# Performance work log

Hardware: AMD Instinct MI355X
Metric: run time of the kernel (lower is better)

## Reference

```python
import jax, jax.numpy as jnp
import numpy as np

B, IN, OUT, LAT, HID = 65536, 1, 512, 128, 2048
COEFFS = (IN + 1) * OUT * 2  # (in+1)*out*n_harmonics*n_eig = 2048

def setup_inputs() -> dict:
    key = jax.random.key(0)
    k = jax.random.split(key, 6)
    x = jax.random.normal(k[0], (B, IN + 1 + LAT), dtype=jnp.float32)
    fc1_w = jax.random.normal(k[1], (LAT, HID), dtype=jnp.float32) * (1.0 / np.sqrt(LAT))
    fc1_b = jax.random.normal(k[2], (HID,), dtype=jnp.float32) * 0.02
    fc2_w = jax.random.normal(k[3], (HID, COEFFS), dtype=jnp.float32) * (1.0 / np.sqrt(HID))
    fc2_b = jax.random.normal(k[4], (COEFFS,), dtype=jnp.float32) * 0.02
    dil = jnp.ones((4,), dtype=jnp.float32)      # dilation1..4
    shift_p = jnp.zeros((4,), dtype=jnp.float32)  # shift1..4
    return {"x": x, "fc1_w": fc1_w, "fc1_b": fc1_b, "fc2_w": fc2_w,
            "fc2_b": fc2_b, "dil": dil, "shift_p": shift_p}

def reference(x, fc1_w, fc1_b, fc2_w, fc2_b, dil, shift_p):
    s = x[-1, IN]                       # scalar time of last sample
    inp = x[:, :IN]                     # [B, 1]
    z = x[:, -LAT:]                     # [B, LAT]
    # CoeffDecoder: tanh MLP
    h = jnp.tanh(z @ fc1_w + fc1_b)     # [B, HID]
    coeffs = (h @ fc2_w + fc2_b).reshape(B, (IN + 1) * OUT, 2)
    # aew trig basis Bin (2x4) has only 4 nonzeros; X.sum(2) == coeffs @ Bin.sum(axis=1)
    t = s * dil + shift_p               # [4]
    v = jnp.stack([jnp.cos(t[0]) + jnp.cos(t[2]),
                   jnp.sin(t[1]) + jnp.sin(t[3])])  # [2] = row-sums of Bin
    w = coeffs @ v                      # [B, (IN+1)*OUT]
    weight = w[:, :IN * OUT].reshape(B, IN, OUT)
    bias = w[:, IN * OUT:(IN + 1) * OUT]
    weighted = jnp.einsum('bi,bio->bo', inp, weight)  # bmm([B,1,1],[B,1,OUT]).squeeze(1)
    return weighted + bias              # [B, OUT]
```

## Files before the change

### kernel.cpp

```cpp
#include <hip/hip_runtime.h>
#include <hip/hip_bf16.h>
#include <stddef.h>

#define NB   65536
#define XC   130
#define LATD 128
#define HIDD 2048
#define JC   1024
#define OC   512
#define BM   128
#define BN   512
#define KCH  32
#define NKC  64

typedef __bf16 bf16_t;
typedef bf16_t bf16x8 __attribute__((ext_vector_type(8)));
typedef float  f32x4  __attribute__((ext_vector_type(4)));

typedef __attribute__((address_space(1))) const unsigned char ga_u8;
typedef __attribute__((address_space(3))) unsigned char ls_u8;

__device__ __forceinline__ void dma16(const void* g, void* l) {
  __builtin_amdgcn_global_load_lds((ga_u8*)g, (ls_u8*)l, 16, 0, 0);
}

__global__ void prep_fc1(const float* __restrict__ fc1w, bf16_t* __restrict__ fc1wT) {
  int t = blockIdx.x * blockDim.x + threadIdx.x;
  int k = t & (LATD - 1);
  int n = t >> 7;
  fc1wT[(size_t)n * LATD + k] = (bf16_t)fc1w[(size_t)k * HIDD + n];
}

__global__ void prep_fc2(const float* __restrict__ x, const float* __restrict__ fc2w,
                         const float* __restrict__ fc2b, const float* __restrict__ dil,
                         const float* __restrict__ shp, bf16_t* __restrict__ w2pT,
                         float* __restrict__ b2p) {
  int t = blockIdx.x * blockDim.x + threadIdx.x;
  int k = t & (HIDD - 1);
  int c = t >> 11;
  float s  = x[(size_t)(NB - 1) * XC + 1];
  float t0 = s * dil[0] + shp[0];
  float t1 = s * dil[1] + shp[1];
  float t2 = s * dil[2] + shp[2];
  float t3 = s * dil[3] + shp[3];
  float v0 = cosf(t0) + cosf(t2);
  float v1 = sinf(t1) + sinf(t3);
  int jj = ((c >> 5) * 16 + (c & 15)) + (((c >> 4) & 1) << 9);
  float w0 = fc2w[(size_t)k * 2048 + 2 * jj];
  float w1 = fc2w[(size_t)k * 2048 + 2 * jj + 1];
  w2pT[(size_t)c * HIDD + k] = (bf16_t)(w0 * v0 + w1 * v1);
  if (k == 0) b2p[c] = fc2b[2 * jj] * v0 + fc2b[2 * jj + 1] * v1;
}

__global__ __launch_bounds__(512, 2) void wag_main(
    const float* __restrict__ x, const float* __restrict__ fc1b,
    const bf16_t* __restrict__ fc1wT, const bf16_t* __restrict__ w2pT,
    const float* __restrict__ b2p, float* __restrict__ out)
{
  __shared__ bf16_t w2t[2][BN * KCH];
  __shared__ bf16_t f1t[2][KCH * LATD];
  __shared__ bf16_t h_lds[BM * 64];
  __shared__ float  inp_lds[BM];

  const int t   = threadIdx.x;
  const int w   = t >> 6;
  const int l   = t & 63;
  const int lhi = l >> 4;
  const int llo = l & 15;
  const size_t b0 = (size_t)blockIdx.x * BM;
  const int    bc = blockIdx.y * BN;

  bf16x8 za[4];
  {
    const float* zsrc = x + (b0 + w * 16 + llo) * XC + 2;
#pragma unroll
    for (int ks = 0; ks < 4; ++ks) {
      bf16x8 pk;
#pragma unroll
      for (int i = 0; i < 4; ++i) {
        float2 f = *(const float2*)(zsrc + ks * 32 + lhi * 8 + 2 * i);
        pk[2 * i]     = (bf16_t)f.x;
        pk[2 * i + 1] = (bf16_t)f.y;
      }
      za[ks] = pk;
    }
    if (t < BM) inp_lds[t] = x[(b0 + t) * XC];
  }

  f32x4 acc[4][8] = {};

  auto stage_w2 = [&](int kc) {
    const int buf = kc & 1;
#pragma unroll
    for (int q = 0; q < 4; ++q) {
      int j   = w * 4 + q;
      int col = j * 16 + (l >> 2);
      const char* src = (const char*)(w2pT + (size_t)(bc + col) * HIDD + kc * KCH + (l & 3) * 8);
      dma16(src, (char*)w2t[buf] + j * 1024);
    }
  };
  auto stage_f1 = [&](int j64, int buf) {
    int col = w * 4 + (l >> 4);
    int kb  = ((l & 15) * 16) ^ ((col & 7) << 4);
    const char* src = (const char*)fc1wT + ((size_t)(j64 * KCH + col) * LATD) * 2 + kb;
    dma16(src, (char*)f1t[buf] + w * 1024);
  };

  auto G1 = [&](int j) {
    const int buf = j & 1;
#pragma unroll
    for (int nt = 0; nt < 2; ++nt) {
      int col = nt * 16 + llo;
      f32x4 c1 = {};
#pragma unroll
      for (int ks = 0; ks < 4; ++ks) {
        int fb = col * 256 + ((ks * 64 + lhi * 16) ^ ((col & 7) << 4));
        bf16x8 b = *(const bf16x8*)((const char*)f1t[buf] + fb);
        c1 = __builtin_amdgcn_mfma_f32_16x16x32_bf16(za[ks], b, c1, 0, 0, 0);
      }
      float bias = fc1b[j * KCH + col];
#pragma unroll
      for (int r = 0; r < 4; ++r) {
        float pre = c1[r] + bias;
        float e   = __builtin_amdgcn_exp2f(pre * 2.88539008177792681f);
        float th  = 1.0f - 2.0f * __builtin_amdgcn_rcpf(e + 1.0f);
        int hr = w * 16 + lhi * 4 + r;
        int hb = (hr * 128 + (buf * KCH + col) * 2) ^ ((hr & 7) << 4);
        *(bf16_t*)((char*)h_lds + hb) = (bf16_t)th;
      }
    }
  };

  auto G2 = [&](int kc) {
    const int buf = kc & 1;
    const int mrb = (w & 1) * 64;
    const int ncb = (w >> 1) * 128;
    bf16x8 a[4];
#pragma unroll
    for (int mt = 0; mt < 4; ++mt) {
      int hr = mrb + mt * 16 + llo;
      a[mt] = *(const bf16x8*)((const char*)h_lds +
               (hr * 128 + ((buf * 64 + lhi * 16) ^ ((hr & 7) << 4))));
    }
    __builtin_amdgcn_s_setprio(1);
#pragma unroll
    for (int nt = 0; nt < 8; ++nt) {
      int col = ncb + nt * 16 + llo;
      bf16x8 b = *(const bf16x8*)((const char*)w2t[buf] + (col * 64 + lhi * 16));
#pragma unroll
      for (int mt = 0; mt < 4; ++mt)
        acc[mt][nt] = __builtin_amdgcn_mfma_f32_16x16x32_bf16(a[mt], b, acc[mt][nt], 0, 0, 0);
    }
    __builtin_amdgcn_s_setprio(0);
  };

  stage_f1(0, 0);
  stage_w2(0);
  __syncthreads();
  stage_f1(1, 1);
  G1(0);
  __syncthreads();

  for (int kc = 0; kc < NKC; ++kc) {
    if (kc < NKC - 1) stage_w2(kc + 1);
    if (kc < NKC - 2) stage_f1(kc + 2, kc & 1);
    if (kc < NKC - 1) G1(kc + 1);
    G2(kc);
    if (kc < NKC - 1) __syncthreads();
  }

  {
    const int mrb = (w & 1) * 64;
    const int ncb = (w >> 1) * 128;
#pragma unroll
    for (int p = 0; p < 4; ++p) {
      int cw = bc + ncb + p * 32 + llo;
      float bw = b2p[cw];
      float bb = b2p[cw + 16];
      int oc = (bc + ncb + p * 32) / 2 + llo;
#pragma unroll
      for (int mt = 0; mt < 4; ++mt) {
#pragma unroll
        for (int r = 0; r < 4; ++r) {
          int row = mrb + mt * 16 + lhi * 4 + r;
          float wv = acc[mt][2 * p][r] + bw;
          float bv = acc[mt][2 * p + 1][r] + bb;
          out[(b0 + row) * OC + oc] = inp_lds[row] * wv + bv;
        }
      }
    }
  }
}

extern "C" void kernel_launch(void* const* d_in, const int* in_sizes, int n_in,
                              void* d_out, int out_size, void* d_ws, size_t ws_size,
                              hipStream_t stream) {
  const float* x    = (const float*)d_in[0];
  const float* fc1w = (const float*)d_in[1];
  const float* fc1b = (const float*)d_in[2];
  const float* fc2w = (const float*)d_in[3];
  const float* fc2b = (const float*)d_in[4];
  const float* dil  = (const float*)d_in[5];
  const float* shp  = (const float*)d_in[6];
  float* out = (float*)d_out;

  bf16_t* fc1wT = (bf16_t*)d_ws;
  bf16_t* w2pT  = fc1wT + (size_t)HIDD * LATD;
  float*  b2p   = (float*)(w2pT + (size_t)JC * HIDD);

  prep_fc1<<<(HIDD * LATD) / 256, 256, 0, stream>>>(fc1w, fc1wT);
  prep_fc2<<<(JC * HIDD) / 256, 256, 0, stream>>>(x, fc2w, fc2b, dil, shp, w2pT, b2p);
  wag_main<<<dim3(NB / BM, JC / BN), 512, 0, stream>>>(x, fc1b, fc1wT, w2pT, b2p, out);
}
```

Before: 498.4 us.

## Split fused MLP into banded hidden-activation kernel plus GEMM kernel

The fused kernel, which recomputed the first layer (fc1 + tanh) inside each output-column block, is split into two kernels. A separate kernel computes h for a band of 16384 rows and writes it to a bf16 workspace buffer. The second GEMM then streams h through LDS with a new k-major layout. Banding keeps the h buffer small enough to stay cache-resident, and the split removes the duplicated fc1 work across the two column blocks and frees the GEMM loop of tanh computation. In exchange it adds global write and read traffic for h, extra kernel launches, and serial dependencies between bands.

```diff
diff --git a/kernel.cpp b/kernel.cpp
--- a/kernel.cpp
+++ b/kernel.cpp
@@ -12,6 +12,7 @@
 #define BN   512
 #define KCH  32
 #define NKC  64
+#define BAND 16384
 
 typedef __bf16 bf16_t;
 typedef bf16_t bf16x8 __attribute__((ext_vector_type(8)));
@@ -52,23 +53,18 @@
   if (k == 0) b2p[c] = fc2b[2 * jj] * v0 + fc2b[2 * jj + 1] * v1;
 }
 
-__global__ __launch_bounds__(512, 2) void wag_main(
+__global__ __launch_bounds__(256) void h_kernel(
     const float* __restrict__ x, const float* __restrict__ fc1b,
-    const bf16_t* __restrict__ fc1wT, const bf16_t* __restrict__ w2pT,
-    const float* __restrict__ b2p, float* __restrict__ out)
+    const bf16_t* __restrict__ fc1wT, bf16_t* __restrict__ h, int band)
 {
-  __shared__ bf16_t w2t[2][BN * KCH];
-  __shared__ bf16_t f1t[2][KCH * LATD];
-  __shared__ bf16_t h_lds[BM * 64];
-  __shared__ float  inp_lds[BM];
-
+  __shared__ bf16_t tile[4][16 * 64];
   const int t   = threadIdx.x;
   const int w   = t >> 6;
   const int l   = t & 63;
   const int lhi = l >> 4;
   const int llo = l & 15;
-  const size_t b0 = (size_t)blockIdx.x * BM;
-  const int    bc = blockIdx.y * BN;
+  const size_t b0 = (size_t)band * BAND + (size_t)blockIdx.x * 64;
+  const int    hr0 = blockIdx.x * 64 + w * 16;
 
   bf16x8 za[4];
   {
@@ -84,69 +80,93 @@
       }
       za[ks] = pk;
     }
-    if (t < BM) inp_lds[t] = x[(b0 + t) * XC];
-  }
-
-  f32x4 acc[4][8] = {};
-
-  auto stage_w2 = [&](int kc) {
-    const int buf = kc & 1;
-#pragma unroll
-    for (int q = 0; q < 4; ++q) {
-      int j   = w * 4 + q;
-      int col = j * 16 + (l >> 2);
-      const char* src = (const char*)(w2pT + (size_t)(bc + col) * HIDD + kc * KCH + (l & 3) * 8);
-      dma16(src, (char*)w2t[buf] + j * 1024);
-    }
-  };
-  auto stage_f1 = [&](int j64, int buf) {
-    int col = w * 4 + (l >> 4);
-    int kb  = ((l & 15) * 16) ^ ((col & 7) << 4);
-    const char* src = (const char*)fc1wT + ((size_t)(j64 * KCH + col) * LATD) * 2 + kb;
-    dma16(src, (char*)f1t[buf] + w * 1024);
-  };
-
-  auto G1 = [&](int j) {
-    const int buf = j & 1;
-#pragma unroll
-    for (int nt = 0; nt < 2; ++nt) {
-      int col = nt * 16 + llo;
+  }
+
+  for (int j = 0; j < 32; ++j) {
+#pragma unroll
+    for (int nt = 0; nt < 4; ++nt) {
+      int col = j * 64 + nt * 16 + llo;
       f32x4 c1 = {};
 #pragma unroll
       for (int ks = 0; ks < 4; ++ks) {
-        int fb = col * 256 + ((ks * 64 + lhi * 16) ^ ((col & 7) << 4));
-        bf16x8 b = *(const bf16x8*)((const char*)f1t[buf] + fb);
+        bf16x8 b = *(const bf16x8*)(fc1wT + (size_t)col * LATD + ks * 32 + lhi * 8);
         c1 = __builtin_amdgcn_mfma_f32_16x16x32_bf16(za[ks], b, c1, 0, 0, 0);
       }
-      float bias = fc1b[j * KCH + col];
+      float bias = fc1b[col];
 #pragma unroll
       for (int r = 0; r < 4; ++r) {
         float pre = c1[r] + bias;
         float e   = __builtin_amdgcn_exp2f(pre * 2.88539008177792681f);
         float th  = 1.0f - 2.0f * __builtin_amdgcn_rcpf(e + 1.0f);
-        int hr = w * 16 + lhi * 4 + r;
-        int hb = (hr * 128 + (buf * KCH + col) * 2) ^ ((hr & 7) << 4);
-        *(bf16_t*)((char*)h_lds + hb) = (bf16_t)th;
-      }
+        int row = lhi * 4 + r;
+        int tb  = row * 128 + (((nt * 16 + llo) * 2) ^ ((row & 7) << 4));
+        *(bf16_t*)((char*)tile[w] + tb) = (bf16_t)th;
+      }
+    }
+#pragma unroll
+    for (int half = 0; half < 2; ++half) {
+      int row = l >> 2;
+      int rb  = row * 128 + ((((l & 3) * 16) + half * 64) ^ ((row & 7) << 4));
+      bf16x8 v = *(const bf16x8*)((const char*)tile[w] + rb);
+      *(bf16x8*)(h + (size_t)(hr0 + row) * HIDD + j * 64 + (l & 3) * 8 + half * 32) = v;
+    }
+  }
+}
+
+__global__ __launch_bounds__(512, 2) void wag_main(
+    const float* __restrict__ x, const bf16_t* __restrict__ hband,
+    const bf16_t* __restrict__ w2pT, const float* __restrict__ b2p,
+    float* __restrict__ out, int band)
+{
+  __shared__ bf16_t w2t[2][BN * KCH];
+  __shared__ bf16_t ht[2][BM * KCH];
+  __shared__ float  inp_lds[BM];
+
+  const int t   = threadIdx.x;
+  const int w   = t >> 6;
+  const int l   = t & 63;
+  const int lhi = l >> 4;
+  const int llo = l & 15;
+  const size_t b0 = (size_t)band * BAND + (size_t)blockIdx.x * BM;
+  const int    hrow0 = blockIdx.x * BM;
+  const int    bc  = blockIdx.y * BN;
+  const int    mrb = (w & 1) * 64;
+  const int    ncb = (w >> 1) * 128;
+
+  if (t < BM) inp_lds[t] = x[(b0 + t) * XC];
+
+  f32x4 acc[4][8] = {};
+
+  auto stage = [&](int kc) {
+    const int buf = kc & 1;
+#pragma unroll
+    for (int q = 0; q < 4; ++q) {
+      int j  = w * 4 + q;
+      int ks = j >> 3, cb = j & 7;
+      const char* src = (const char*)w2pT +
+          ((size_t)(bc + cb * 64 + l) * HIDD + kc * KCH + ks * 8) * 2;
+      dma16(src, (char*)w2t[buf] + ks * 8192 + cb * 1024 + l * 16);
+    }
+    {
+      int ks = w >> 1, rb = w & 1;
+      const char* src = (const char*)hband +
+          ((size_t)(hrow0 + rb * 64 + l) * HIDD + kc * KCH + ks * 8) * 2;
+      dma16(src, (char*)ht[buf] + ks * 2048 + rb * 1024 + l * 16);
     }
   };
 
   auto G2 = [&](int kc) {
     const int buf = kc & 1;
-    const int mrb = (w & 1) * 64;
-    const int ncb = (w >> 1) * 128;
     bf16x8 a[4];
 #pragma unroll
-    for (int mt = 0; mt < 4; ++mt) {
-      int hr = mrb + mt * 16 + llo;
-      a[mt] = *(const bf16x8*)((const char*)h_lds +
-               (hr * 128 + ((buf * 64 + lhi * 16) ^ ((hr & 7) << 4))));
-    }
+    for (int mt = 0; mt < 4; ++mt)
+      a[mt] = *(const bf16x8*)((const char*)ht[buf] +
+               (lhi * 2048 + (mrb + mt * 16 + llo) * 16));
     __builtin_amdgcn_s_setprio(1);
 #pragma unroll
     for (int nt = 0; nt < 8; ++nt) {
-      int col = ncb + nt * 16 + llo;
-      bf16x8 b = *(const bf16x8*)((const char*)w2t[buf] + (col * 64 + lhi * 16));
+      bf16x8 b = *(const bf16x8*)((const char*)w2t[buf] +
+                 (lhi * 8192 + (ncb + nt * 16 + llo) * 16));
 #pragma unroll
       for (int mt = 0; mt < 4; ++mt)
         acc[mt][nt] = __builtin_amdgcn_mfma_f32_16x16x32_bf16(a[mt], b, acc[mt][nt], 0, 0, 0);
@@ -154,39 +174,28 @@
     __builtin_amdgcn_s_setprio(0);
   };
 
-  stage_f1(0, 0);
-  stage_w2(0);
+  stage(0);
   __syncthreads();
-  stage_f1(1, 1);
-  G1(0);
-  __syncthreads();
-
   for (int kc = 0; kc < NKC; ++kc) {
-    if (kc < NKC - 1) stage_w2(kc + 1);
-    if (kc < NKC - 2) stage_f1(kc + 2, kc & 1);
-    if (kc < NKC - 1) G1(kc + 1);
+    if (kc < NKC - 1) stage(kc + 1);
     G2(kc);
     if (kc < NKC - 1) __syncthreads();
   }
 
-  {
-    const int mrb = (w & 1) * 64;
-    const int ncb = (w >> 1) * 128;
-#pragma unroll
-    for (int p = 0; p < 4; ++p) {
-      int cw = bc + ncb + p * 32 + llo;
-      float bw = b2p[cw];
-      float bb = b2p[cw + 16];
-      int oc = (bc + ncb + p * 32) / 2 + llo;
-#pragma unroll
-      for (int mt = 0; mt < 4; ++mt) {
-#pragma unroll
-        for (int r = 0; r < 4; ++r) {
-          int row = mrb + mt * 16 + lhi * 4 + r;
-          float wv = acc[mt][2 * p][r] + bw;
-          float bv = acc[mt][2 * p + 1][r] + bb;
-          out[(b0 + row) * OC + oc] = inp_lds[row] * wv + bv;
-        }
+#pragma unroll
+  for (int p = 0; p < 4; ++p) {
+    int cw = bc + ncb + p * 32 + llo;
+    float bw = b2p[cw];
+    float bb = b2p[cw + 16];
+    int oc = (bc + ncb + p * 32) / 2 + llo;
+#pragma unroll
+    for (int mt = 0; mt < 4; ++mt) {
+#pragma unroll
+      for (int r = 0; r < 4; ++r) {
+        int row = mrb + mt * 16 + lhi * 4 + r;
+        float wv = acc[mt][2 * p][r] + bw;
+        float bv = acc[mt][2 * p + 1][r] + bb;
+        out[(b0 + row) * OC + oc] = inp_lds[row] * wv + bv;
       }
     }
   }
@@ -207,8 +216,13 @@
   bf16_t* fc1wT = (bf16_t*)d_ws;
   bf16_t* w2pT  = fc1wT + (size_t)HIDD * LATD;
   float*  b2p   = (float*)(w2pT + (size_t)JC * HIDD);
+  bf16_t* hband = (bf16_t*)((char*)d_ws + ((512 * 1024) + (4 * 1024 * 1024) + 65536));
 
   prep_fc1<<<(HIDD * LATD) / 256, 256, 0, stream>>>(fc1w, fc1wT);
   prep_fc2<<<(JC * HIDD) / 256, 256, 0, stream>>>(x, fc2w, fc2b, dil, shp, w2pT, b2p);
-  wag_main<<<dim3(NB / BM, JC / BN), 512, 0, stream>>>(x, fc1b, fc1wT, w2pT, b2p, out);
-}
+
+  for (int band = 0; band < NB / BAND; ++band) {
+    h_kernel<<<BAND / 64, 256, 0, stream>>>(x, fc1b, fc1wT, hband, band);
+    wag_main<<<dim3(BAND / BM, JC / BN), 512, 0, stream>>>(x, hband, w2pT, b2p, out, band);
+  }
+}
```

Measured after the change: 905.3 us. 81.6% more time.

## Restructure fused MLP pipeline: register fc1 operands, triple-buffered W2, k-major LDS layout

Applied to the files above, without the earlier changes.

The first GEMM now takes fc1 weights straight from global memory into registers as the A operand, with z as the B operand. This removes the fc1 LDS staging and lets each wave compute a 16x32 slice of h. W2 tiles are triple-buffered with a k-major LDS layout, and h is double-buffered in a compact k-major layout. The loop is unrolled by two with manual vmcnt waits and raw barriers, so DMA loads stay in flight across iterations and sync stalls shrink. The fc1 bias is cached in LDS. The risks are higher register pressure from the extra A and za arrays, possible LDS bank conflicts in the new unswizzled layouts, and fragile hand-counted waitcnt values.

```diff
diff --git a/kernel.cpp b/kernel.cpp
--- a/kernel.cpp
+++ b/kernel.cpp
@@ -14,6 +14,7 @@
 #define NKC  64
 
 typedef __bf16 bf16_t;
+typedef bf16_t bf16x4 __attribute__((ext_vector_type(4)));
 typedef bf16_t bf16x8 __attribute__((ext_vector_type(8)));
 typedef float  f32x4  __attribute__((ext_vector_type(4)));
 
@@ -57,9 +58,9 @@
     const bf16_t* __restrict__ fc1wT, const bf16_t* __restrict__ w2pT,
     const float* __restrict__ b2p, float* __restrict__ out)
 {
-  __shared__ bf16_t w2t[2][BN * KCH];
-  __shared__ bf16_t f1t[2][KCH * LATD];
-  __shared__ bf16_t h_lds[BM * 64];
+  __shared__ bf16_t w2t[3][BN * KCH];
+  __shared__ bf16_t ht[2][BM * KCH];
+  __shared__ float  fb_lds[HIDD];
   __shared__ float  inp_lds[BM];
 
   const int t   = threadIdx.x;
@@ -68,11 +69,19 @@
   const int lhi = l >> 4;
   const int llo = l & 15;
   const size_t b0 = (size_t)blockIdx.x * BM;
-  const int    bc = blockIdx.y * BN;
-
-  bf16x8 za[4];
-  {
-    const float* zsrc = x + (b0 + w * 16 + llo) * XC + 2;
+  const int    bc  = blockIdx.y * BN;
+  const int    hb  = w & 1;
+  const int    gb  = (w >> 1) * 32;
+  const int    mrb = (w & 1) * 64;
+  const int    ncb = (w >> 1) * 128;
+
+  ((float4*)fb_lds)[t] = ((const float4*)fc1b)[t];
+  if (t < BM) inp_lds[t] = x[(b0 + t) * XC];
+
+  bf16x8 za[2][4];
+#pragma unroll
+  for (int bb2 = 0; bb2 < 2; ++bb2) {
+    const float* zsrc = x + (b0 + gb + bb2 * 16 + llo) * XC + 2;
 #pragma unroll
     for (int ks = 0; ks < 4; ++ks) {
       bf16x8 pk;
@@ -82,71 +91,63 @@
         pk[2 * i]     = (bf16_t)f.x;
         pk[2 * i + 1] = (bf16_t)f.y;
       }
-      za[ks] = pk;
-    }
-    if (t < BM) inp_lds[t] = x[(b0 + t) * XC];
+      za[bb2][ks] = pk;
+    }
   }
 
   f32x4 acc[4][8] = {};
 
   auto stage_w2 = [&](int kc) {
-    const int buf = kc & 1;
+    const int buf = kc % 3;
 #pragma unroll
     for (int q = 0; q < 4; ++q) {
-      int j   = w * 4 + q;
-      int col = j * 16 + (l >> 2);
-      const char* src = (const char*)(w2pT + (size_t)(bc + col) * HIDD + kc * KCH + (l & 3) * 8);
-      dma16(src, (char*)w2t[buf] + j * 1024);
-    }
-  };
-  auto stage_f1 = [&](int j64, int buf) {
-    int col = w * 4 + (l >> 4);
-    int kb  = ((l & 15) * 16) ^ ((col & 7) << 4);
-    const char* src = (const char*)fc1wT + ((size_t)(j64 * KCH + col) * LATD) * 2 + kb;
-    dma16(src, (char*)f1t[buf] + w * 1024);
-  };
-
-  auto G1 = [&](int j) {
-    const int buf = j & 1;
-#pragma unroll
-    for (int nt = 0; nt < 2; ++nt) {
-      int col = nt * 16 + llo;
+      int j  = w * 4 + q;
+      int ks = j >> 3, cb = j & 7;
+      const char* src = (const char*)w2pT +
+          ((size_t)(bc + cb * 64 + l) * HIDD + kc * KCH + ks * 8) * 2;
+      dma16(src, (char*)w2t[buf] + ks * 8192 + cb * 1024 + l * 16);
+    }
+  };
+
+  auto loadA = [&](bf16x8 (&A)[4], int j) {
+    const bf16_t* base = fc1wT + (size_t)(j * KCH + hb * 16 + llo) * LATD + lhi * 8;
+#pragma unroll
+    for (int ks = 0; ks < 4; ++ks) A[ks] = *(const bf16x8*)(base + ks * 32);
+  };
+
+  auto G1 = [&](int j, bf16x8 (&A)[4]) {
+    float4 fb = *(const float4*)(&fb_lds[j * KCH + hb * 16 + lhi * 4]);
+#pragma unroll
+    for (int bb2 = 0; bb2 < 2; ++bb2) {
       f32x4 c1 = {};
 #pragma unroll
-      for (int ks = 0; ks < 4; ++ks) {
-        int fb = col * 256 + ((ks * 64 + lhi * 16) ^ ((col & 7) << 4));
-        bf16x8 b = *(const bf16x8*)((const char*)f1t[buf] + fb);
-        c1 = __builtin_amdgcn_mfma_f32_16x16x32_bf16(za[ks], b, c1, 0, 0, 0);
-      }
-      float bias = fc1b[j * KCH + col];
+      for (int ks = 0; ks < 4; ++ks)
+        c1 = __builtin_amdgcn_mfma_f32_16x16x32_bf16(A[ks], za[bb2][ks], c1, 0, 0, 0);
+      bf16x4 pk;
 #pragma unroll
       for (int r = 0; r < 4; ++r) {
-        float pre = c1[r] + bias;
+        float pre = c1[r] + ((const float*)&fb)[r];
         float e   = __builtin_amdgcn_exp2f(pre * 2.88539008177792681f);
         float th  = 1.0f - 2.0f * __builtin_amdgcn_rcpf(e + 1.0f);
-        int hr = w * 16 + lhi * 4 + r;
-        int hb = (hr * 128 + (buf * KCH + col) * 2) ^ ((hr & 7) << 4);
-        *(bf16_t*)((char*)h_lds + hb) = (bf16_t)th;
+        pk[r] = (bf16_t)th;
       }
+      int row = gb + bb2 * 16 + llo;
+      int off = (hb * 2 + (lhi >> 1)) * 2048 + row * 16 + (lhi & 1) * 8;
+      *(bf16x4*)((char*)ht[j & 1] + off) = pk;
     }
   };
 
   auto G2 = [&](int kc) {
-    const int buf = kc & 1;
-    const int mrb = (w & 1) * 64;
-    const int ncb = (w >> 1) * 128;
+    const char* hbuf = (const char*)ht[kc & 1];
+    const char* wbuf = (const char*)w2t[kc % 3];
     bf16x8 a[4];
 #pragma unroll
-    for (int mt = 0; mt < 4; ++mt) {
-      int hr = mrb + mt * 16 + llo;
-      a[mt] = *(const bf16x8*)((const char*)h_lds +
-               (hr * 128 + ((buf * 64 + lhi * 16) ^ ((hr & 7) << 4))));
-    }
+    for (int mt = 0; mt < 4; ++mt)
+      a[mt] = *(const bf16x8*)(hbuf + lhi * 2048 + (mrb + mt * 16 + llo) * 16);
     __builtin_amdgcn_s_setprio(1);
 #pragma unroll
     for (int nt = 0; nt < 8; ++nt) {
-      int col = ncb + nt * 16 + llo;
-      bf16x8 b = *(const bf16x8*)((const char*)w2t[buf] + (col * 64 + lhi * 16));
+      bf16x8 b = *(const bf16x8*)(wbuf + lhi * 8192 + (ncb + nt * 16 + llo) * 16);
 #pragma unroll
       for (int mt = 0; mt < 4; ++mt)
         acc[mt][nt] = __builtin_amdgcn_mfma_f32_16x16x32_bf16(a[mt], b, acc[mt][nt], 0, 0, 0);
@@ -154,39 +155,49 @@
     __builtin_amdgcn_s_setprio(0);
   };
 
-  stage_f1(0, 0);
+  bf16x8 A0[4], A1[4];
   stage_w2(0);
+  stage_w2(1);
+  loadA(A0, 0);
+  loadA(A1, 1);
   __syncthreads();
-  stage_f1(1, 1);
-  G1(0);
+  G1(0, A0);
   __syncthreads();
 
-  for (int kc = 0; kc < NKC; ++kc) {
-    if (kc < NKC - 1) stage_w2(kc + 1);
-    if (kc < NKC - 2) stage_f1(kc + 2, kc & 1);
-    if (kc < NKC - 1) G1(kc + 1);
+  for (int kc = 0; kc < 62; kc += 2) {
+    stage_w2(kc + 2);
+    loadA(A0, kc + 2);
+    G1(kc + 1, A1);
     G2(kc);
-    if (kc < NKC - 1) __syncthreads();
+    asm volatile("s_waitcnt vmcnt(8) lgkmcnt(0)" ::: "memory");
+    __builtin_amdgcn_s_barrier();
+    stage_w2(kc + 3);
+    loadA(A1, kc + 3);
+    G1(kc + 2, A0);
+    G2(kc + 1);
+    asm volatile("s_waitcnt vmcnt(8) lgkmcnt(0)" ::: "memory");
+    __builtin_amdgcn_s_barrier();
   }
-
-  {
-    const int mrb = (w & 1) * 64;
-    const int ncb = (w >> 1) * 128;
-#pragma unroll
-    for (int p = 0; p < 4; ++p) {
-      int cw = bc + ncb + p * 32 + llo;
-      float bw = b2p[cw];
-      float bb = b2p[cw + 16];
-      int oc = (bc + ncb + p * 32) / 2 + llo;
-#pragma unroll
-      for (int mt = 0; mt < 4; ++mt) {
-#pragma unroll
-        for (int r = 0; r < 4; ++r) {
-          int row = mrb + mt * 16 + lhi * 4 + r;
-          float wv = acc[mt][2 * p][r] + bw;
-          float bv = acc[mt][2 * p + 1][r] + bb;
-          out[(b0 + row) * OC + oc] = inp_lds[row] * wv + bv;
-        }
+  G1(63, A1);
+  G2(62);
+  asm volatile("s_waitcnt vmcnt(0) lgkmcnt(0)" ::: "memory");
+  __builtin_amdgcn_s_barrier();
+  G2(63);
+
+#pragma unroll
+  for (int p = 0; p < 4; ++p) {
+    int cw = bc + ncb + p * 32 + llo;
+    float bw = b2p[cw];
+    float bb = b2p[cw + 16];
+    int oc = (bc + ncb + p * 32) / 2 + llo;
+#pragma unroll
+    for (int mt = 0; mt < 4; ++mt) {
+#pragma unroll
+      for (int r = 0; r < 4; ++r) {
+        int row = mrb + mt * 16 + lhi * 4 + r;
+        float wv = acc[mt][2 * p][r] + bw;
+        float bv = acc[mt][2 * p + 1][r] + bb;
+        out[(b0 + row) * OC + oc] = inp_lds[row] * wv + bv;
       }
     }
   }
```

Measured after the change: 696.3 us. +39.7%, slower.
